# Performance work log

Hardware: AMD Instinct MI355X
Metric: run time of the kernel (lower is better)

## Reference

```python
import jax, jax.numpy as jnp
import numpy as np
from jax import lax

B, T_ENC, T_DEC = 32, 256, 256
N_MEL = 80
MEM_D = 768
ATT_RNN = 1024
DEC_RNN = 1024
PRENET = 256
ATT_D = 128
NF = 32
K = 31
PAD = (K - 1) // 2


def setup_inputs() -> dict:
    key = jax.random.key(0)
    ks = jax.random.split(key, 20)
    def w(k, shape, fan_in):
        return jax.random.normal(k, shape, jnp.float32) / np.sqrt(fan_in).astype(np.float32)
    inp = {}
    inp['memory'] = jax.random.normal(ks[0], (B, T_ENC, MEM_D), jnp.float32)
    inp['decoder_inputs'] = jax.random.normal(ks[1], (T_DEC, B, N_MEL), jnp.float32)
    inp['mask'] = jnp.zeros((B, T_ENC), bool)
    inp['prenet_W1'] = w(ks[2], (PRENET, N_MEL), N_MEL)
    inp['prenet_W2'] = w(ks[3], (PRENET, PRENET), PRENET)
    att_in = PRENET + MEM_D
    inp['att_Wih'] = w(ks[4], (4 * ATT_RNN, att_in), att_in)
    inp['att_Whh'] = w(ks[5], (4 * ATT_RNN, ATT_RNN), ATT_RNN)
    inp['att_bih'] = jnp.zeros((4 * ATT_RNN,), jnp.float32)
    inp['att_bhh'] = jnp.zeros((4 * ATT_RNN,), jnp.float32)
    inp['query_W'] = w(ks[6], (ATT_D, ATT_RNN), ATT_RNN)
    inp['memory_W'] = w(ks[7], (ATT_D, MEM_D), MEM_D)
    inp['v_W'] = w(ks[8], (1, ATT_D), ATT_D)
    inp['loc_conv_W'] = w(ks[9], (NF, 2, K), 2 * K)
    inp['loc_dense_W'] = w(ks[10], (ATT_D, NF), NF)
    dec_in = ATT_RNN + MEM_D
    inp['dec_Wih'] = w(ks[11], (4 * DEC_RNN, dec_in), dec_in)
    inp['dec_Whh'] = w(ks[12], (4 * DEC_RNN, DEC_RNN), DEC_RNN)
    inp['dec_bih'] = jnp.zeros((4 * DEC_RNN,), jnp.float32)
    inp['dec_bhh'] = jnp.zeros((4 * DEC_RNN,), jnp.float32)
    proj_in = DEC_RNN + MEM_D
    inp['proj_W'] = w(ks[13], (N_MEL, proj_in), proj_in)
    inp['proj_b'] = jnp.zeros((N_MEL,), jnp.float32)
    inp['gate_W'] = w(ks[14], (1, proj_in), proj_in)
    inp['gate_b'] = jnp.zeros((1,), jnp.float32)
    return inp


def _lstm_cell(x, h, c, Wih, Whh, bih, bhh):
    gates = x @ Wih.T + h @ Whh.T + (bih + bhh)
    i, f, g, o = jnp.split(gates, 4, axis=-1)
    c2 = jax.nn.sigmoid(f) * c + jax.nn.sigmoid(i) * jnp.tanh(g)
    h2 = jax.nn.sigmoid(o) * jnp.tanh(c2)
    return h2, c2


def _decode(memory, decoder_inputs, mask, prenet_W1, prenet_W2,
            att_Wih, att_Whh, att_bih, att_bhh,
            query_W, memory_W, v_W, loc_conv_W, loc_dense_W,
            dec_Wih, dec_Whh, dec_bih, dec_bhh,
            proj_W, proj_b, gate_W, gate_b):
    # teacher forcing: inputs are [go_frame, target[:-1]]
    go = jnp.zeros((1, B, N_MEL), decoder_inputs.dtype)
    x = jnp.concatenate([go, decoder_inputs[:-1]], axis=0)  # [T_DEC, B, N_MEL]
    # prenet (no dropout, p=0): two relu linears, bias=False
    x = jax.nn.relu(x @ prenet_W1.T)
    x = jax.nn.relu(x @ prenet_W2.T)  # [T_DEC, B, PRENET]
    processed_memory = memory @ memory_W.T  # [B, T_ENC, ATT_D]
    v = v_W[0]  # [ATT_D]

    def step(carry, x_t):
        att_h, att_c, dec_h, dec_c, aw, aw_cum, ctx = carry
        cell_in = jnp.concatenate([x_t, ctx], axis=-1)
        att_h, att_c = _lstm_cell(cell_in, att_h, att_c, att_Wih, att_Whh, att_bih, att_bhh)
        # location-sensitive attention
        awc = jnp.stack([aw, aw_cum], axis=1)  # [B, 2, T_ENC]
        loc = lax.conv_general_dilated(awc, loc_conv_W, window_strides=(1,),
                                       padding=[(PAD, PAD)],
                                       dimension_numbers=('NCH', 'OIH', 'NCH'))  # [B, NF, T_ENC]
        processed = jnp.einsum('bft,af->bta', loc, loc_dense_W)  # [B, T_ENC, ATT_D]
        query = att_h @ query_W.T  # [B, ATT_D]
        energies = jnp.einsum('bta,a->bt', jnp.tanh(processed + query[:, None, :] + processed_memory), v)
        energies = jnp.where(mask, -jnp.inf, energies)
        aw = jax.nn.softmax(energies, axis=1)  # [B, T_ENC]
        ctx = jnp.einsum('bt,btd->bd', aw, memory)  # [B, MEM_D]
        aw_cum = aw_cum + aw
        dec_in = jnp.concatenate([att_h, ctx], axis=-1)
        dec_h, dec_c = _lstm_cell(dec_in, dec_h, dec_c, dec_Wih, dec_Whh, dec_bih, dec_bhh)
        proj_in = jnp.concatenate([dec_h, ctx], axis=-1)
        mel = proj_in @ proj_W.T + proj_b  # [B, N_MEL]
        gate = (proj_in @ gate_W.T + gate_b)[:, 0]  # [B]
        return (att_h, att_c, dec_h, dec_c, aw, aw_cum, ctx), (mel, gate, aw)

    f32 = memory.dtype
    carry0 = (jnp.zeros((B, ATT_RNN), f32), jnp.zeros((B, ATT_RNN), f32),
              jnp.zeros((B, DEC_RNN), f32), jnp.zeros((B, DEC_RNN), f32),
              jnp.zeros((B, T_ENC), f32), jnp.zeros((B, T_ENC), f32),
              jnp.zeros((B, MEM_D), f32))
    _, (mels, gates, aligns) = lax.scan(step, carry0, x)
    # [B, T_DEC, N_MEL], [B, T_DEC], [B, T_DEC, T_ENC]
    return mels.transpose(1, 0, 2), gates.T, aligns.transpose(1, 0, 2)


def reference(memory, decoder_inputs, mask, prenet_W1, prenet_W2,
              att_Wih, att_Whh, att_bih, att_bhh,
              query_W, memory_W, v_W, loc_conv_W, loc_dense_W,
              dec_Wih, dec_Whh, dec_bih, dec_bhh,
              proj_W, proj_b, gate_W, gate_b):
    return _decode(memory, decoder_inputs, mask, prenet_W1, prenet_W2,
                   att_Wih, att_Whh, att_bih, att_bhh,
                   query_W, memory_W, v_W, loc_conv_W, loc_dense_W,
                   dec_Wih, dec_Whh, dec_bih, dec_bhh,
                   proj_W, proj_b, gate_W, gate_b)
```

## Files before the change

kernel.cpp:

```cpp
#include <hip/hip_runtime.h>
#include <cstddef>

#define TB   32
#define TENC 256
#define TDEC 256
#define NMEL 80
#define MEMD 768
#define ARNN 1024
#define PRN  256
#define ATTD 128
#define NFLT 32
#define KSZ  31
#define KPAD 15
#define SSTR 260

__device__ __forceinline__ float sigf(float x){ return 1.f/(1.f+expf(-x)); }

__global__ __launch_bounds__(256) void k_prenet1(const float* __restrict__ din,
                                                 const float* __restrict__ W1,
                                                 float* __restrict__ out){
  const int row = blockIdx.x;
  const int t = row >> 5, b = row & 31;
  const int tid = threadIdx.x;
  __shared__ float x[NMEL];
  if (tid < NMEL) x[tid] = (t == 0) ? 0.f : din[((size_t)(t-1)*TB + b)*NMEL + tid];
  __syncthreads();
  const float* wr = W1 + (size_t)tid*NMEL;
  float s = 0.f;
  #pragma unroll
  for (int m = 0; m < NMEL; ++m) s += x[m]*wr[m];
  out[(size_t)row*PRN + tid] = fmaxf(s, 0.f);
}

__global__ __launch_bounds__(256) void k_prenet2(float* __restrict__ buf,
                                                 const float* __restrict__ W2){
  const int row = blockIdx.x;
  const int tid = threadIdx.x;
  __shared__ float x[PRN];
  x[tid] = buf[(size_t)row*PRN + tid];
  __syncthreads();
  const float4* wr = (const float4*)(W2 + (size_t)tid*PRN);
  const float4* xx = (const float4*)x;
  float s = 0.f;
  #pragma unroll 8
  for (int k = 0; k < PRN/4; ++k) {
    float4 w = wr[k], v = xx[k];
    s += w.x*v.x + w.y*v.y + w.z*v.z + w.w*v.w;
  }
  buf[(size_t)row*PRN + tid] = fmaxf(s, 0.f);
}

__global__ __launch_bounds__(128) void k_procmem(const float* __restrict__ mem,
                                                 const float* __restrict__ mW,
                                                 float* __restrict__ pm){
  const int row = blockIdx.x;
  const int tid = threadIdx.x;
  __shared__ float x[MEMD];
  for (int i = tid; i < MEMD; i += 128) x[i] = mem[(size_t)row*MEMD + i];
  __syncthreads();
  const float4* wr = (const float4*)(mW + (size_t)tid*MEMD);
  const float4* xx = (const float4*)x;
  float s = 0.f;
  #pragma unroll 8
  for (int k = 0; k < MEMD/4; ++k) {
    float4 w = wr[k], v = xx[k];
    s += w.x*v.x + w.y*v.y + w.z*v.z + w.w*v.w;
  }
  pm[(size_t)row*ATTD + tid] = s;
}

__device__ __forceinline__ void lstm_body(int bi, int tid,
    float* smem, float* ldsg,
    const float* __restrict__ in1, int L1,
    const float* __restrict__ in2, int L2,
    const float* __restrict__ hbm,
    const float* __restrict__ Wih, const float* __restrict__ Whh,
    const float* __restrict__ bih, const float* __restrict__ bhh,
    const float* __restrict__ cT_in, float* cT_out, float* h_bm_out)
{
  const int Kin = L1 + L2, Ktot = Kin + ARNN;
  const int w = tid >> 6, lane = tid & 63;
  const int r = lane >> 4, kl = lane & 15;
  const int u = w >> 1, bh = w & 1, b0 = bh*16;
  const int j = bi*2 + u;
  float acc[16];
  #pragma unroll
  for (int b = 0; b < 16; ++b) acc[b] = 0.f;

  for (int kc = 0; kc < Ktot; kc += 256) {
    const float* src; int kq, Ls;
    if (kc < L1)       { src = in1; kq = kc;       Ls = L1; }
    else if (kc < Kin) { src = in2; kq = kc - L1;  Ls = L2; }
    else               { src = hbm; kq = kc - Kin; Ls = ARNN; }
    const float* Wb; int rs, kof;
    if (kc < Kin) { Wb = Wih; rs = Kin;  kof = kc; }
    else          { Wb = Whh; rs = ARNN; kof = kc - Kin; }
    const float* wr = Wb + (size_t)(r*ARNN + j)*rs + kof;
    const float4 wv0 = *(const float4*)(wr + (0*16 + kl)*4);
    const float4 wv1 = *(const float4*)(wr + (1*16 + kl)*4);
    const float4 wv2 = *(const float4*)(wr + (2*16 + kl)*4);
    const float4 wv3 = *(const float4*)(wr + (3*16 + kl)*4);
    __syncthreads();
    #pragma unroll
    for (int tc = 0; tc < 8; ++tc) {
      const int f4 = tid + tc*256;
      const int bb = f4 >> 6, k4 = f4 & 63;
      *(float4*)(&smem[bb*SSTR + k4*4]) =
          *(const float4*)(src + (size_t)bb*Ls + kq + k4*4);
    }
    __syncthreads();
    #pragma unroll
    for (int b = 0; b < 16; ++b) {
      const float* sb = &smem[(b0 + b)*SSTR + kl*4];
      const float4 s0 = *(const float4*)(sb + 0*64);
      const float4 s1 = *(const float4*)(sb + 1*64);
      const float4 s2 = *(const float4*)(sb + 2*64);
      const float4 s3 = *(const float4*)(sb + 3*64);
      float a = acc[b];
      a = fmaf(wv0.x,s0.x, fmaf(wv0.y,s0.y, fmaf(wv0.z,s0.z, fmaf(wv0.w,s0.w, a))));
      a = fmaf(wv1.x,s1.x, fmaf(wv1.y,s1.y, fmaf(wv1.z,s1.z, fmaf(wv1.w,s1.w, a))));
      a = fmaf(wv2.x,s2.x, fmaf(wv2.y,s2.y, fmaf(wv2.z,s2.z, fmaf(wv2.w,s2.w, a))));
      a = fmaf(wv3.x,s3.x, fmaf(wv3.y,s3.y, fmaf(wv3.z,s3.z, fmaf(wv3.w,s3.w, a))));
      acc[b] = a;
    }
  }
  #pragma unroll
  for (int b = 0; b < 16; ++b) {
    acc[b] += __shfl_xor(acc[b], 1);
    acc[b] += __shfl_xor(acc[b], 2);
    acc[b] += __shfl_xor(acc[b], 4);
    acc[b] += __shfl_xor(acc[b], 8);
  }
  if (kl == 0) {
    #pragma unroll
    for (int b = 0; b < 16; ++b) ldsg[(w*4 + r)*17 + b] = acc[b];
  }
  if (lane < 16) {
    const int b = b0 + lane;
    const float gi = ldsg[(w*4 + 0)*17 + lane] + bih[j]          + bhh[j];
    const float gf = ldsg[(w*4 + 1)*17 + lane] + bih[ARNN + j]   + bhh[ARNN + j];
    const float gg = ldsg[(w*4 + 2)*17 + lane] + bih[2*ARNN + j] + bhh[2*ARNN + j];
    const float go = ldsg[(w*4 + 3)*17 + lane] + bih[3*ARNN + j] + bhh[3*ARNN + j];
    const float c  = sigf(gf)*cT_in[j*32 + b] + sigf(gi)*tanhf(gg);
    const float h  = sigf(go)*tanhf(c);
    cT_out[j*32 + b] = c;
    h_bm_out[(size_t)b*ARNN + j] = h;
  }
}

__device__ __forceinline__ void eterm_body(int eb, int tid, float* smem,
    const float* __restrict__ aw_prev, int awp_stride,
    const float* __restrict__ aw_cum,
    const float* __restrict__ conv_W, const float* __restrict__ dense_W,
    const float* __restrict__ pm, float* __restrict__ eterm)
{
  const int b   = eb >> 3;
  const int te0 = (eb & 7)*32;
  float* awp = smem;
  float* awc = smem + 64;
  float* cw  = smem + 128;
  float* loc = smem + 2112;
  if (tid < 62) {
    const int te = te0 - KPAD + tid;
    const bool ok = (te >= 0) && (te < TENC);
    awp[tid] = ok ? aw_prev[(size_t)b*awp_stride + te] : 0.f;
    awc[tid] = ok ? aw_cum[(size_t)b*TENC + te] : 0.f;
  }
  for (int i = tid; i < NFLT*2*KSZ; i += 256) cw[i] = conv_W[i];
  __syncthreads();
  {
    const int te = tid & 31;
    const int fq = tid >> 5;
    #pragma unroll
    for (int ff = 0; ff < 4; ++ff) {
      const int f = fq*4 + ff;
      const float* wf = cw + f*2*KSZ;
      float s = 0.f;
      #pragma unroll
      for (int kk = 0; kk < KSZ; ++kk) s += awp[te+kk]*wf[kk];
      #pragma unroll
      for (int kk = 0; kk < KSZ; ++kk) s += awc[te+kk]*wf[KSZ+kk];
      loc[f*33 + te] = s;
    }
  }
  __syncthreads();
  {
    const int a  = tid & 127;
    const int th = tid >> 7;
    float la[NFLT];
    const float* lr = dense_W + (size_t)a*NFLT;
    #pragma unroll
    for (int f = 0; f < NFLT; ++f) la[f] = lr[f];
    #pragma unroll
    for (int t4 = 0; t4 < 16; ++t4) {
      const int tel = th*16 + t4;
      const int te = te0 + tel;
      float accv = pm[((size_t)b*TENC + te)*ATTD + a];
      #pragma unroll 8
      for (int f = 0; f < NFLT; ++f) accv = fmaf(la[f], loc[f*33 + tel], accv);
      eterm[((size_t)b*TENC + te)*ATTD + a] = accv;
    }
  }
}

__global__ __launch_bounds__(256, 4) void k_step(
    int tA, int nab, int neb,
    const float* __restrict__ xp, const float* __restrict__ cx,
    float* ahbm2, float* acT, float* dhbm, float* dcT,
    const float* __restrict__ aWih, const float* __restrict__ aWhh,
    const float* __restrict__ abih, const float* __restrict__ abhh,
    const float* __restrict__ dWih, const float* __restrict__ dWhh,
    const float* __restrict__ dbih, const float* __restrict__ dbhh,
    const float* __restrict__ aw0, const float* __restrict__ out_al,
    const float* __restrict__ awcum,
    const float* __restrict__ cvW, const float* __restrict__ ldW,
    const float* __restrict__ pm, float* __restrict__ et)
{
  __shared__ float smem[32*SSTR];
  __shared__ float ldsg[4*4*17];
  int bi = blockIdx.x;
  const int tid = threadIdx.x;
  if (bi < nab) {
    const int cur = tA & 1, nxt = cur ^ 1;
    lstm_body(bi, tid, smem, ldsg,
        xp + (size_t)tA*TB*PRN, PRN,
        cx + (size_t)tA*TB*MEMD, MEMD,
        ahbm2 + (size_t)cur*TB*ARNN,
        aWih, aWhh, abih, abhh,
        acT + (size_t)cur*ARNN*TB, acT + (size_t)nxt*ARNN*TB,
        ahbm2 + (size_t)nxt*TB*ARNN);
    return;
  }
  bi -= nab;
  if (bi < neb) {
    const float* awprev = (tA == 0) ? aw0 : (out_al + (size_t)(tA-1)*TENC);
    const int awps = (tA == 0) ? TENC : TDEC*TENC;
    eterm_body(bi, tid, smem, awprev, awps, awcum, cvW, ldW, pm, et);
    return;
  }
  bi -= neb;
  {
    const int tD = tA - 1;
    const int curD = tD & 1, nxtD = curD ^ 1;
    lstm_body(bi, tid, smem, ldsg,
        ahbm2 + (size_t)nxtD*TB*ARNN, ARNN,
        cx + (size_t)(tD+1)*TB*MEMD, MEMD,
        dhbm + (size_t)tD*TB*ARNN,
        dWih, dWhh, dbih, dbhh,
        dcT + (size_t)curD*ARNN*TB, dcT + (size_t)nxtD*ARNN*TB,
        dhbm + (size_t)(tD+1)*TB*ARNN);
  }
}

__global__ __launch_bounds__(512) void k_attn(
    const float* __restrict__ att_h,
    const float* __restrict__ query_W,
    const float* __restrict__ v_W,
    const float* __restrict__ eterm,
    float* __restrict__ aw_out, int awo_stride,
    float* __restrict__ aw_cum,
    const float* __restrict__ mem,
    float* __restrict__ ctx_out)
{
  const int b = blockIdx.x;
  const int tid = threadIdx.x;
  __shared__ float hrow[ARNN];
  __shared__ float qp[512];
  __shared__ float q[ATTD];
  __shared__ float vv[ATTD];
  __shared__ float aws[TENC];
  __shared__ float red[16];
  __shared__ float ctxp[192*4];
  if (tid < 256) ((float4*)hrow)[tid] = ((const float4*)(att_h + (size_t)b*ARNN))[tid];
  if (tid < ATTD) vv[tid] = v_W[tid];
  __syncthreads();
  {
    const int a = tid & 127, kh = tid >> 7;
    const float4* wr = (const float4*)(query_W + (size_t)a*ARNN + kh*256);
    const float4* xx = (const float4*)(hrow + kh*256);
    float s = 0.f;
    #pragma unroll 8
    for (int k = 0; k < 64; ++k) {
      float4 w = wr[k], x = xx[k];
      s += w.x*x.x + w.y*x.y + w.z*x.z + w.w*x.w;
    }
    qp[tid] = s;
  }
  __syncthreads();
  if (tid < ATTD) q[tid] = qp[tid] + qp[128 + tid] + qp[256 + tid] + qp[384 + tid];
  __syncthreads();
  float e = 0.f;
  {
    const int te = tid >> 1, ah = tid & 1;
    const float* et = eterm + ((size_t)b*TENC + te)*ATTD + ah*64;
    const float* qq = q + ah*64;
    const float* vq = vv + ah*64;
    #pragma unroll 4
    for (int a4 = 0; a4 < 16; ++a4) {
      float4 t4 = *(const float4*)(et + a4*4);
      e += vq[a4*4+0]*tanhf(qq[a4*4+0] + t4.x);
      e += vq[a4*4+1]*tanhf(qq[a4*4+1] + t4.y);
      e += vq[a4*4+2]*tanhf(qq[a4*4+2] + t4.z);
      e += vq[a4*4+3]*tanhf(qq[a4*4+3] + t4.w);
    }
    e += __shfl_xor(e, 1, 64);
  }
  float m1 = e;
  #pragma unroll
  for (int d = 1; d < 64; d <<= 1) m1 = fmaxf(m1, __shfl_xor(m1, d, 64));
  if ((tid & 63) == 0) red[tid >> 6] = m1;
  __syncthreads();
  float mx = red[0];
  #pragma unroll
  for (int i = 1; i < 8; ++i) mx = fmaxf(mx, red[i]);
  const float p = expf(e - mx);
  float s1 = ((tid & 1) == 0) ? p : 0.f;
  #pragma unroll
  for (int d = 1; d < 64; d <<= 1) s1 += __shfl_xor(s1, d, 64);
  if ((tid & 63) == 0) red[8 + (tid >> 6)] = s1;
  __syncthreads();
  float sden = red[8];
  #pragma unroll
  for (int i = 1; i < 8; ++i) sden += red[8 + i];
  const float aw = p / sden;
  if ((tid & 1) == 0) {
    const int te = tid >> 1;
    aw_out[(size_t)b*awo_stride + te] = aw;
    aw_cum[(size_t)b*TENC + te] += aw;
    aws[te] = aw;
  }
  __syncthreads();
  if (tid < 384) {
    const int th = tid / 192;
    const int d4 = tid % 192;
    const float* mc = mem + (size_t)b*TENC*MEMD + (size_t)th*128*MEMD + d4*4;
    const float* aa = aws + th*128;
    float4 s4 = make_float4(0.f, 0.f, 0.f, 0.f);
    #pragma unroll 8
    for (int te = 0; te < 128; ++te) {
      float4 m4 = *(const float4*)(mc + (size_t)te*MEMD);
      const float a = aa[te];
      s4.x = fmaf(a, m4.x, s4.x); s4.y = fmaf(a, m4.y, s4.y);
      s4.z = fmaf(a, m4.z, s4.z); s4.w = fmaf(a, m4.w, s4.w);
    }
    if (th == 1) *(float4*)(&ctxp[d4*4]) = s4;
    __syncthreads();
    if (th == 0) {
      const float4 o4 = *(const float4*)(&ctxp[d4*4]);
      s4.x += o4.x; s4.y += o4.y; s4.z += o4.z; s4.w += o4.w;
      *(float4*)(ctx_out + (size_t)b*MEMD + d4*4) = s4;
    }
  } else {
    __syncthreads();
  }
}

__global__ __launch_bounds__(192) void k_proj(
    const float* __restrict__ dh_all,
    const float* __restrict__ cx_all,
    const float* __restrict__ proj_W,
    const float* __restrict__ proj_b,
    const float* __restrict__ gate_W,
    const float* __restrict__ gate_b,
    float* __restrict__ out_mel,
    float* __restrict__ out_gate)
{
  const int b = blockIdx.y;
  const int tid = threadIdx.x;
  __shared__ float pin[ARNN + MEMD];
  __shared__ float pp[192];
  for (int t0 = 0; t0 < 32; ++t0) {
    const int t = blockIdx.x*32 + t0;
    __syncthreads();
    for (int i = tid; i < 448; i += 192) {
      float4 v;
      if (i < 256) v = *(const float4*)(dh_all + ((size_t)(t+1)*TB + b)*ARNN + i*4);
      else         v = *(const float4*)(cx_all + ((size_t)(t+1)*TB + b)*MEMD + (i-256)*4);
      *(float4*)(&pin[i*4]) = v;
    }
    __syncthreads();
    if (tid < 160) {
      const int m = tid >> 1, kh = tid & 1;
      const float4* wr = (const float4*)(proj_W + (size_t)m*1792 + kh*896);
      const float4* xx = (const float4*)(pin + kh*896);
      float s = 0.f;
      #pragma unroll 8
      for (int k = 0; k < 224; ++k) {
        float4 w = wr[k], x = xx[k];
        s += w.x*x.x + w.y*x.y + w.z*x.z + w.w*x.w;
      }
      pp[tid] = s;
    } else if (tid == 160) {
      const float4* wr = (const float4*)gate_W;
      const float4* xx = (const float4*)pin;
      float s = 0.f;
      #pragma unroll 8
      for (int k = 0; k < 448; ++k) {
        float4 w = wr[k], x = xx[k];
        s += w.x*x.x + w.y*x.y + w.z*x.z + w.w*x.w;
      }
      out_gate[(size_t)b*TDEC + t] = s + gate_b[0];
    }
    __syncthreads();
    if (tid < NMEL) out_mel[((size_t)b*TDEC + t)*NMEL + tid] = pp[2*tid] + pp[2*tid+1] + proj_b[tid];
  }
}

extern "C" void kernel_launch(void* const* d_in, const int* in_sizes, int n_in,
                              void* d_out, int out_size, void* d_ws, size_t ws_size,
                              hipStream_t stream) {
  const float* mem  = (const float*)d_in[0];
  const float* din  = (const float*)d_in[1];
  const float* pW1  = (const float*)d_in[3];
  const float* pW2  = (const float*)d_in[4];
  const float* aWih = (const float*)d_in[5];
  const float* aWhh = (const float*)d_in[6];
  const float* abih = (const float*)d_in[7];
  const float* abhh = (const float*)d_in[8];
  const float* qW   = (const float*)d_in[9];
  const float* mW   = (const float*)d_in[10];
  const float* vW   = (const float*)d_in[11];
  const float* cvW  = (const float*)d_in[12];
  const float* ldW  = (const float*)d_in[13];
  const float* dWih = (const float*)d_in[14];
  const float* dWhh = (const float*)d_in[15];
  const float* dbih = (const float*)d_in[16];
  const float* dbhh = (const float*)d_in[17];
  const float* prW  = (const float*)d_in[18];
  const float* prb  = (const float*)d_in[19];
  const float* gW   = (const float*)d_in[20];
  const float* gb   = (const float*)d_in[21];

  float* ws = (float*)d_ws;
  size_t o = 0;
  float* xp    = ws + o; o += (size_t)TDEC*TB*PRN;
  float* pm    = ws + o; o += (size_t)TB*TENC*ATTD;
  float* et    = ws + o; o += (size_t)TB*TENC*ATTD;
  float* acT   = ws + o; o += (size_t)2*ARNN*TB;
  float* dcT   = ws + o; o += (size_t)2*ARNN*TB;
  float* ahbm2 = ws + o; o += (size_t)2*TB*ARNN;
  float* dhbm  = ws + o; o += (size_t)(TDEC+1)*TB*ARNN;
  float* cx    = ws + o; o += (size_t)(TDEC+1)*TB*MEMD;
  float* awcum = ws + o; o += (size_t)TB*TENC;
  float* aw0   = ws + o; o += (size_t)TB*TENC;
  if (ws_size < o*sizeof(float)) return;

  float* out_mel  = (float*)d_out;
  float* out_gate = out_mel + (size_t)TB*TDEC*NMEL;
  float* out_al   = out_gate + (size_t)TB*TDEC;

  (void)hipMemsetAsync(acT, 0, (size_t)2*ARNN*TB*sizeof(float), stream);
  (void)hipMemsetAsync(dcT, 0, (size_t)2*ARNN*TB*sizeof(float), stream);
  (void)hipMemsetAsync(ahbm2, 0, (size_t)2*TB*ARNN*sizeof(float), stream);
  (void)hipMemsetAsync(dhbm, 0, (size_t)TB*ARNN*sizeof(float), stream);
  (void)hipMemsetAsync(cx, 0, (size_t)TB*MEMD*sizeof(float), stream);
  (void)hipMemsetAsync(awcum, 0, (size_t)TB*TENC*sizeof(float), stream);
  (void)hipMemsetAsync(aw0, 0, (size_t)TB*TENC*sizeof(float), stream);

  k_prenet1<<<TDEC*TB, 256, 0, stream>>>(din, pW1, xp);
  k_prenet2<<<TDEC*TB, 256, 0, stream>>>(xp, pW2);
  k_procmem<<<TB*TENC, 128, 0, stream>>>(mem, mW, pm);

  k_step<<<512 + 256, 256, 0, stream>>>(
      0, 512, 256, xp, cx, ahbm2, acT, dhbm, dcT,
      aWih, aWhh, abih, abhh, dWih, dWhh, dbih, dbhh,
      aw0, out_al, awcum, cvW, ldW, pm, et);

  for (int t = 0; t < TDEC; ++t) {
    const int nxt = (t & 1) ^ 1;
    k_attn<<<TB, 512, 0, stream>>>(
        ahbm2 + (size_t)nxt*TB*ARNN, qW, vW, et,
        out_al + (size_t)t*TENC, TDEC*TENC, awcum,
        mem, cx + (size_t)(t+1)*TB*MEMD);
    if (t < TDEC - 1) {
      k_step<<<512 + 256 + 512, 256, 0, stream>>>(
          t + 1, 512, 256, xp, cx, ahbm2, acT, dhbm, dcT,
          aWih, aWhh, abih, abhh, dWih, dWhh, dbih, dbhh,
          aw0, out_al, awcum, cvW, ldW, pm, et);
    } else {
      k_step<<<512, 256, 0, stream>>>(
          TDEC, 0, 0, xp, cx, ahbm2, acT, dhbm, dcT,
          aWih, aWhh, abih, abhh, dWih, dWhh, dbih, dbhh,
          aw0, out_al, awcum, cvW, ldW, pm, et);
    }
  }
  k_proj<<<dim3(8, TB), 192, 0, stream>>>(dhbm, cx, prW, prb, gW, gb, out_mel, out_gate);
}
```

Baseline: 22.66 ms.

## Fuse attention into step kernel with atomic counters for intra-launch dependency

Removes the separate per-step attention launch and moves attention into the step kernel as extra blocks. These blocks spin on per-step atomic counters until the attention-LSTM and location-energy blocks of the same launch have finished. This halves the number of launches in the sequential loop and lets decoder-LSTM work overlap with attention. In exchange it relies on forward-progress assumptions for spin-waiting blocks, which could deadlock if the waiting blocks occupy the CUs first. Attention now runs on 256 threads per batch row instead of 512, so each block does more serial work.

Result: slower. 33.95 ms (+49.8%).

```diff
diff --git a/kernel.cpp b/kernel.cpp
--- a/kernel.cpp
+++ b/kernel.cpp
@@ -13,6 +13,10 @@
 #define KSZ  31
 #define KPAD 15
 #define SSTR 260
+#define NAB  512
+#define NEB  256
+#define NCB  512
+#define NATT 32
 
 __device__ __forceinline__ float sigf(float x){ return 1.f/(1.f+expf(-x)); }
 
@@ -203,25 +207,101 @@
   }
 }
 
+__device__ __forceinline__ void attn_body(int b, int tid, float* smem, int t,
+    const float* __restrict__ att_h, const float* __restrict__ query_W,
+    const float* __restrict__ v_W, const float* __restrict__ eterm,
+    float* __restrict__ out_al, float* __restrict__ aw_cum,
+    const float* __restrict__ mem, float* __restrict__ ctx_out)
+{
+  float* hrow = smem;
+  float* qp   = smem + 1024;
+  float* q    = smem + 1280;
+  float* vv   = smem + 1408;
+  float* aws  = smem + 1536;
+  float* red  = smem + 1792;
+  ((float4*)hrow)[tid] = ((const float4*)(att_h + (size_t)b*ARNN))[tid];
+  if (tid < ATTD) vv[tid] = v_W[tid];
+  __syncthreads();
+  {
+    const int a = tid & 127, kh = tid >> 7;
+    const float4* wr = (const float4*)(query_W + (size_t)a*ARNN + kh*512);
+    const float4* xx = (const float4*)(hrow + kh*512);
+    float s = 0.f;
+    #pragma unroll 8
+    for (int k = 0; k < 128; ++k) {
+      float4 w = wr[k], x = xx[k];
+      s += w.x*x.x + w.y*x.y + w.z*x.z + w.w*x.w;
+    }
+    qp[tid] = s;
+  }
+  __syncthreads();
+  if (tid < ATTD) q[tid] = qp[tid] + qp[128 + tid];
+  __syncthreads();
+  float e = 0.f;
+  {
+    const float* etr = eterm + ((size_t)b*TENC + tid)*ATTD;
+    #pragma unroll 8
+    for (int a4 = 0; a4 < 32; ++a4) {
+      float4 t4 = *(const float4*)(etr + a4*4);
+      e += vv[a4*4+0]*tanhf(q[a4*4+0] + t4.x);
+      e += vv[a4*4+1]*tanhf(q[a4*4+1] + t4.y);
+      e += vv[a4*4+2]*tanhf(q[a4*4+2] + t4.z);
+      e += vv[a4*4+3]*tanhf(q[a4*4+3] + t4.w);
+    }
+  }
+  float m1 = e;
+  #pragma unroll
+  for (int d = 1; d < 64; d <<= 1) m1 = fmaxf(m1, __shfl_xor(m1, d, 64));
+  if ((tid & 63) == 0) red[tid >> 6] = m1;
+  __syncthreads();
+  const float mx = fmaxf(fmaxf(red[0], red[1]), fmaxf(red[2], red[3]));
+  const float p = expf(e - mx);
+  float s1 = p;
+  #pragma unroll
+  for (int d = 1; d < 64; d <<= 1) s1 += __shfl_xor(s1, d, 64);
+  if ((tid & 63) == 0) red[4 + (tid >> 6)] = s1;
+  __syncthreads();
+  const float sden = red[4] + red[5] + red[6] + red[7];
+  const float aw = p / sden;
+  out_al[(size_t)b*TDEC*TENC + (size_t)t*TENC + tid] = aw;
+  aw_cum[(size_t)b*TENC + tid] += aw;
+  aws[tid] = aw;
+  __syncthreads();
+  if (tid < 192) {
+    const float* mc = mem + (size_t)b*TENC*MEMD + tid*4;
+    float4 s4 = make_float4(0.f, 0.f, 0.f, 0.f);
+    #pragma unroll 8
+    for (int te = 0; te < 256; ++te) {
+      float4 m4 = *(const float4*)(mc + (size_t)te*MEMD);
+      const float a = aws[te];
+      s4.x = fmaf(a, m4.x, s4.x); s4.y = fmaf(a, m4.y, s4.y);
+      s4.z = fmaf(a, m4.z, s4.z); s4.w = fmaf(a, m4.w, s4.w);
+    }
+    *(float4*)(ctx_out + (size_t)b*MEMD + tid*4) = s4;
+  }
+}
+
 __global__ __launch_bounds__(256, 4) void k_step(
-    int tA, int nab, int neb,
-    const float* __restrict__ xp, const float* __restrict__ cx,
+    int tA, int nab, int neb, int ncb,
+    const float* __restrict__ xp, float* cx,
     float* ahbm2, float* acT, float* dhbm, float* dcT,
     const float* __restrict__ aWih, const float* __restrict__ aWhh,
     const float* __restrict__ abih, const float* __restrict__ abhh,
     const float* __restrict__ dWih, const float* __restrict__ dWhh,
     const float* __restrict__ dbih, const float* __restrict__ dbhh,
-    const float* __restrict__ aw0, const float* __restrict__ out_al,
-    const float* __restrict__ awcum,
+    const float* __restrict__ aw0, float* out_al, float* awcum,
     const float* __restrict__ cvW, const float* __restrict__ ldW,
-    const float* __restrict__ pm, float* __restrict__ et)
+    const float* __restrict__ pm, float* __restrict__ et,
+    const float* __restrict__ qW, const float* __restrict__ vW,
+    const float* __restrict__ mem,
+    unsigned* cntA, unsigned* cntE)
 {
   __shared__ float smem[32*SSTR];
   __shared__ float ldsg[4*4*17];
   int bi = blockIdx.x;
   const int tid = threadIdx.x;
+  const int cur = tA & 1, nxt = cur ^ 1;
   if (bi < nab) {
-    const int cur = tA & 1, nxt = cur ^ 1;
     lstm_body(bi, tid, smem, ldsg,
         xp + (size_t)tA*TB*PRN, PRN,
         cx + (size_t)tA*TB*MEMD, MEMD,
@@ -229,6 +309,11 @@
         aWih, aWhh, abih, abhh,
         acT + (size_t)cur*ARNN*TB, acT + (size_t)nxt*ARNN*TB,
         ahbm2 + (size_t)nxt*TB*ARNN);
+    __syncthreads();
+    if (tid == 0) {
+      __threadfence();
+      __hip_atomic_fetch_add(&cntA[tA], 1u, __ATOMIC_RELEASE, __HIP_MEMORY_SCOPE_AGENT);
+    }
     return;
   }
   bi -= nab;
@@ -236,10 +321,16 @@
     const float* awprev = (tA == 0) ? aw0 : (out_al + (size_t)(tA-1)*TENC);
     const int awps = (tA == 0) ? TENC : TDEC*TENC;
     eterm_body(bi, tid, smem, awprev, awps, awcum, cvW, ldW, pm, et);
+    __syncthreads();
+    if (tid == 0) {
+      __threadfence();
+      __hip_atomic_fetch_add(&cntE[tA], 1u, __ATOMIC_RELEASE, __HIP_MEMORY_SCOPE_AGENT);
+    }
     return;
   }
   bi -= neb;
-  {
+  if (bi < ncb) {
+    if (tA == 0) return;
     const int tD = tA - 1;
     const int curD = tD & 1, nxtD = curD ^ 1;
     lstm_body(bi, tid, smem, ldsg,
@@ -249,110 +340,20 @@
         dWih, dWhh, dbih, dbhh,
         dcT + (size_t)curD*ARNN*TB, dcT + (size_t)nxtD*ARNN*TB,
         dhbm + (size_t)(tD+1)*TB*ARNN);
-  }
-}
-
-__global__ __launch_bounds__(512) void k_attn(
-    const float* __restrict__ att_h,
-    const float* __restrict__ query_W,
-    const float* __restrict__ v_W,
-    const float* __restrict__ eterm,
-    float* __restrict__ aw_out, int awo_stride,
-    float* __restrict__ aw_cum,
-    const float* __restrict__ mem,
-    float* __restrict__ ctx_out)
-{
-  const int b = blockIdx.x;
-  const int tid = threadIdx.x;
-  __shared__ float hrow[ARNN];
-  __shared__ float qp[512];
-  __shared__ float q[ATTD];
-  __shared__ float vv[ATTD];
-  __shared__ float aws[TENC];
-  __shared__ float red[16];
-  __shared__ float ctxp[192*4];
-  if (tid < 256) ((float4*)hrow)[tid] = ((const float4*)(att_h + (size_t)b*ARNN))[tid];
-  if (tid < ATTD) vv[tid] = v_W[tid];
-  __syncthreads();
-  {
-    const int a = tid & 127, kh = tid >> 7;
-    const float4* wr = (const float4*)(query_W + (size_t)a*ARNN + kh*256);
-    const float4* xx = (const float4*)(hrow + kh*256);
-    float s = 0.f;
-    #pragma unroll 8
-    for (int k = 0; k < 64; ++k) {
-      float4 w = wr[k], x = xx[k];
-      s += w.x*x.x + w.y*x.y + w.z*x.z + w.w*x.w;
-    }
-    qp[tid] = s;
-  }
-  __syncthreads();
-  if (tid < ATTD) q[tid] = qp[tid] + qp[128 + tid] + qp[256 + tid] + qp[384 + tid];
-  __syncthreads();
-  float e = 0.f;
-  {
-    const int te = tid >> 1, ah = tid & 1;
-    const float* et = eterm + ((size_t)b*TENC + te)*ATTD + ah*64;
-    const float* qq = q + ah*64;
-    const float* vq = vv + ah*64;
-    #pragma unroll 4
-    for (int a4 = 0; a4 < 16; ++a4) {
-      float4 t4 = *(const float4*)(et + a4*4);
-      e += vq[a4*4+0]*tanhf(qq[a4*4+0] + t4.x);
-      e += vq[a4*4+1]*tanhf(qq[a4*4+1] + t4.y);
-      e += vq[a4*4+2]*tanhf(qq[a4*4+2] + t4.z);
-      e += vq[a4*4+3]*tanhf(qq[a4*4+3] + t4.w);
-    }
-    e += __shfl_xor(e, 1, 64);
-  }
-  float m1 = e;
-  #pragma unroll
-  for (int d = 1; d < 64; d <<= 1) m1 = fmaxf(m1, __shfl_xor(m1, d, 64));
-  if ((tid & 63) == 0) red[tid >> 6] = m1;
-  __syncthreads();
-  float mx = red[0];
-  #pragma unroll
-  for (int i = 1; i < 8; ++i) mx = fmaxf(mx, red[i]);
-  const float p = expf(e - mx);
-  float s1 = ((tid & 1) == 0) ? p : 0.f;
-  #pragma unroll
-  for (int d = 1; d < 64; d <<= 1) s1 += __shfl_xor(s1, d, 64);
-  if ((tid & 63) == 0) red[8 + (tid >> 6)] = s1;
-  __syncthreads();
-  float sden = red[8];
-  #pragma unroll
-  for (int i = 1; i < 8; ++i) sden += red[8 + i];
-  const float aw = p / sden;
-  if ((tid & 1) == 0) {
-    const int te = tid >> 1;
-    aw_out[(size_t)b*awo_stride + te] = aw;
-    aw_cum[(size_t)b*TENC + te] += aw;
-    aws[te] = aw;
-  }
-  __syncthreads();
-  if (tid < 384) {
-    const int th = tid / 192;
-    const int d4 = tid % 192;
-    const float* mc = mem + (size_t)b*TENC*MEMD + (size_t)th*128*MEMD + d4*4;
-    const float* aa = aws + th*128;
-    float4 s4 = make_float4(0.f, 0.f, 0.f, 0.f);
-    #pragma unroll 8
-    for (int te = 0; te < 128; ++te) {
-      float4 m4 = *(const float4*)(mc + (size_t)te*MEMD);
-      const float a = aa[te];
-      s4.x = fmaf(a, m4.x, s4.x); s4.y = fmaf(a, m4.y, s4.y);
-      s4.z = fmaf(a, m4.z, s4.z); s4.w = fmaf(a, m4.w, s4.w);
-    }
-    if (th == 1) *(float4*)(&ctxp[d4*4]) = s4;
-    __syncthreads();
-    if (th == 0) {
-      const float4 o4 = *(const float4*)(&ctxp[d4*4]);
-      s4.x += o4.x; s4.y += o4.y; s4.z += o4.z; s4.w += o4.w;
-      *(float4*)(ctx_out + (size_t)b*MEMD + d4*4) = s4;
-    }
-  } else {
-    __syncthreads();
-  }
+    return;
+  }
+  bi -= ncb;
+  if (tid == 0) {
+    while (__hip_atomic_load(&cntA[tA], __ATOMIC_ACQUIRE, __HIP_MEMORY_SCOPE_AGENT)
+           < (unsigned)nab) __builtin_amdgcn_s_sleep(4);
+    while (__hip_atomic_load(&cntE[tA], __ATOMIC_ACQUIRE, __HIP_MEMORY_SCOPE_AGENT)
+           < (unsigned)neb) __builtin_amdgcn_s_sleep(4);
+    __threadfence();
+  }
+  __syncthreads();
+  attn_body(bi, tid, smem, tA,
+      ahbm2 + (size_t)nxt*TB*ARNN, qW, vW, et,
+      out_al, awcum, mem, cx + (size_t)(tA+1)*TB*MEMD);
 }
 
 __global__ __launch_bounds__(192) void k_proj(
@@ -440,9 +441,11 @@
   float* dcT   = ws + o; o += (size_t)2*ARNN*TB;
   float* ahbm2 = ws + o; o += (size_t)2*TB*ARNN;
   float* dhbm  = ws + o; o += (size_t)(TDEC+1)*TB*ARNN;
-  float* cx    = ws + o; o += (size_t)(TDEC+1)*TB*MEMD;
+  float* cx    = ws + o; o += (size_t)(TDEC+2)*TB*MEMD;
   float* awcum = ws + o; o += (size_t)TB*TENC;
   float* aw0   = ws + o; o += (size_t)TB*TENC;
+  unsigned* cntA = (unsigned*)(ws + o); o += TDEC;
+  unsigned* cntE = (unsigned*)(ws + o); o += TDEC;
   if (ws_size < o*sizeof(float)) return;
 
   float* out_mel  = (float*)d_out;
@@ -456,33 +459,26 @@
   (void)hipMemsetAsync(cx, 0, (size_t)TB*MEMD*sizeof(float), stream);
   (void)hipMemsetAsync(awcum, 0, (size_t)TB*TENC*sizeof(float), stream);
   (void)hipMemsetAsync(aw0, 0, (size_t)TB*TENC*sizeof(float), stream);
+  (void)hipMemsetAsync(cntA, 0, (size_t)2*TDEC*sizeof(unsigned), stream);
 
   k_prenet1<<<TDEC*TB, 256, 0, stream>>>(din, pW1, xp);
   k_prenet2<<<TDEC*TB, 256, 0, stream>>>(xp, pW2);
   k_procmem<<<TB*TENC, 128, 0, stream>>>(mem, mW, pm);
 
-  k_step<<<512 + 256, 256, 0, stream>>>(
-      0, 512, 256, xp, cx, ahbm2, acT, dhbm, dcT,
+  for (int t = 0; t < TDEC; ++t) {
+    k_step<<<NAB + NEB + NCB + NATT, 256, 0, stream>>>(
+        t, NAB, NEB, NCB,
+        xp, cx, ahbm2, acT, dhbm, dcT,
+        aWih, aWhh, abih, abhh, dWih, dWhh, dbih, dbhh,
+        aw0, out_al, awcum, cvW, ldW, pm, et, qW, vW, mem,
+        cntA, cntE);
+  }
+  k_step<<<NCB, 256, 0, stream>>>(
+      TDEC, 0, 0, NCB,
+      xp, cx, ahbm2, acT, dhbm, dcT,
       aWih, aWhh, abih, abhh, dWih, dWhh, dbih, dbhh,
-      aw0, out_al, awcum, cvW, ldW, pm, et);
-
-  for (int t = 0; t < TDEC; ++t) {
-    const int nxt = (t & 1) ^ 1;
-    k_attn<<<TB, 512, 0, stream>>>(
-        ahbm2 + (size_t)nxt*TB*ARNN, qW, vW, et,
-        out_al + (size_t)t*TENC, TDEC*TENC, awcum,
-        mem, cx + (size_t)(t+1)*TB*MEMD);
-    if (t < TDEC - 1) {
-      k_step<<<512 + 256 + 512, 256, 0, stream>>>(
-          t + 1, 512, 256, xp, cx, ahbm2, acT, dhbm, dcT,
-          aWih, aWhh, abih, abhh, dWih, dWhh, dbih, dbhh,
-          aw0, out_al, awcum, cvW, ldW, pm, et);
-    } else {
-      k_step<<<512, 256, 0, stream>>>(
-          TDEC, 0, 0, xp, cx, ahbm2, acT, dhbm, dcT,
-          aWih, aWhh, abih, abhh, dWih, dWhh, dbih, dbhh,
-          aw0, out_al, awcum, cvW, ldW, pm, et);
-    }
-  }
+      aw0, out_al, awcum, cvW, ldW, pm, et, qW, vW, mem,
+      cntA, cntE);
+
   k_proj<<<dim3(8, TB), 192, 0, stream>>>(dhbm, cx, prW, prb, gW, gb, out_mel, out_gate);
 }
```
